# Kernel optimization log

Hardware: AMD Instinct MI355X
Metric: run time of the kernel (lower is better)

The kernel has to match this reference:

```python
import jax, jax.numpy as jnp
import numpy as np

VIEW_NUM = 360
CHAN_NUM = 512
BATCH = 2
IMG = 512


def setup_inputs() -> dict:
    key = jax.random.key(0)
    x = jax.random.normal(key, (BATCH, 1, IMG, IMG), dtype=jnp.float32)
    return {"x": x}


def _bilinear_sample_zeros(img, ix, iy):
    """Bilinear sample img (B,1,H,W) at pixel coords ix, iy (H,W), zeros padding.
    Matches F.grid_sample(mode='bilinear', padding_mode='zeros', align_corners=False)."""
    H, W = img.shape[-2], img.shape[-1]
    x0 = jnp.floor(ix)
    y0 = jnp.floor(iy)
    x1 = x0 + 1.0
    y1 = y0 + 1.0
    wx1 = ix - x0
    wx0 = 1.0 - wx1
    wy1 = iy - y0
    wy0 = 1.0 - wy1

    def gather(yy, xx):
        valid = (xx >= 0) & (xx <= W - 1) & (yy >= 0) & (yy <= H - 1)
        xi = jnp.clip(xx, 0, W - 1).astype(jnp.int32)
        yi = jnp.clip(yy, 0, H - 1).astype(jnp.int32)
        # fancy-index over spatial dims -> (B,1,H,W)
        return img[:, :, yi, xi] * valid.astype(img.dtype)

    return (gather(y0, x0) * (wy0 * wx0)
            + gather(y0, x1) * (wy0 * wx1)
            + gather(y1, x0) * (wy1 * wx0)
            + gather(y1, x1) * (wy1 * wx1))


def _fp(x):
    B, C, H, W = x.shape
    # affine_grid base coords, align_corners=False: (2i+1)/N - 1
    bx = (2.0 * jnp.arange(W, dtype=x.dtype) + 1.0) / W - 1.0
    by = (2.0 * jnp.arange(H, dtype=x.dtype) + 1.0) / H - 1.0
    X = bx[None, :]  # (1,W)
    Y = by[:, None]  # (H,1)
    i = jnp.arange(VIEW_NUM, dtype=x.dtype)
    angles = -jnp.pi * (i + 1.0) / VIEW_NUM - jnp.pi
    cosv = jnp.cos(angles)
    sinv = jnp.sin(angles)

    def per_view(carry, cs):
        c, s = cs
        # theta = [[c,-s,0],[s,c,0]]; grid = base @ theta^T
        gx = c * X - s * Y  # (H,W) normalized sample x
        gy = s * X + c * Y  # (H,W) normalized sample y
        # unnormalize (align_corners=False)
        ix = ((gx + 1.0) * W - 1.0) * 0.5
        iy = ((gy + 1.0) * H - 1.0) * 0.5
        samp = _bilinear_sample_zeros(x, ix, iy)  # (B,1,H,W)
        return carry, jnp.sum(samp, axis=2)  # sum over height -> (B,1,W)

    _, cols = jax.lax.scan(per_view, 0, (cosv, sinv))  # (V,B,1,W)
    sino = jnp.transpose(cols, (1, 2, 3, 0)) * 0.5  # (B,1,chanNum,viewNum)
    return sino


def reference(x):
    return _fp(x)
```

## Files before the change

### kernel.cpp

```cpp
#include <hip/hip_runtime.h>

typedef __fp16 h2 __attribute__((ext_vector_type(2)));

constexpr int VIEWS = 360;
constexpr int IMGSZ = 512;
constexpr int WCHUNK = 64;
constexpr int KH = 64;
constexpr int NXF4 = 25;
constexpr int PITCH = 100;
constexpr int MAXNY = 94;
constexpr int PW = 712;
constexpr int PH = 704;
constexpr int PAD = 96;

__global__ __launch_bounds__(256) void pad_kernel(const float* __restrict__ x,
                                                  unsigned* __restrict__ padq) {
    constexpr int PW4 = PW / 4;
    constexpr int total = PH * PW4;
    int idx = blockIdx.x * 256 + threadIdx.x;
    if (idx >= total) return;
    int py = idx / PW4;
    int px4 = idx - py * PW4;
    int gx = px4 * 4 - PAD;
    int gy = py - PAD;
    const float* img0 = x;
    const float* img1 = x + (size_t)IMGSZ * IMGSZ;
    float4 a = make_float4(0.f, 0.f, 0.f, 0.f);
    float4 bq = a;
    if ((unsigned)gy < (unsigned)IMGSZ && (unsigned)gx < (unsigned)IMGSZ) {
        size_t off = (size_t)gy * IMGSZ + gx;
        a  = *(const float4*)(img0 + off);
        bq = *(const float4*)(img1 + off);
    }
    uint4 d;
    d.x = __builtin_bit_cast(unsigned, __builtin_amdgcn_cvt_pkrtz(a.x, bq.x));
    d.y = __builtin_bit_cast(unsigned, __builtin_amdgcn_cvt_pkrtz(a.y, bq.y));
    d.z = __builtin_bit_cast(unsigned, __builtin_amdgcn_cvt_pkrtz(a.z, bq.z));
    d.w = __builtin_bit_cast(unsigned, __builtin_amdgcn_cvt_pkrtz(a.w, bq.w));
    *(uint4*)&padq[(size_t)idx * 4] = d;
}

__global__ __launch_bounds__(256) void fp_kernel(const unsigned* __restrict__ padq,
                                                 float* __restrict__ out) {
    __shared__ __align__(16) unsigned tileU[PITCH * MAXNY];

    int blk = blockIdx.x;
    int wc = blk & 7;
    int v = blk >> 3;

    int tid = threadIdx.x;
    int lane = tid & 63;
    int g = tid >> 6;
    int w = wc * WCHUNK + lane;

    double ang = -3.14159265358979323846 * (double)(v + 1) / (double)VIEWS
                 - 3.14159265358979323846;
    float c = (float)cos(ang);
    float s = (float)sin(ang);

    float xw = (float)w + 0.5f - 256.0f;
    float cxw = fmaf(c, xw, 255.5f);
    float sxw = fmaf(s, xw, 255.5f);

    float lo = -1e30f, hi = 1e30f;
    {
        float coef = -s, base = cxw;
        if (fabsf(coef) > 1e-6f) {
            float a = (-1.0f - base) / coef;
            float bq = (512.0f - base) / coef;
            lo = fmaxf(lo, fminf(a, bq));
            hi = fminf(hi, fmaxf(a, bq));
        } else if (!(base > -1.0f && base < 512.0f)) {
            lo = 1e30f; hi = -1e30f;
        }
    }
    {
        float coef = c, base = sxw;
        if (fabsf(coef) > 1e-6f) {
            float a = (-1.0f - base) / coef;
            float bq = (512.0f - base) / coef;
            lo = fmaxf(lo, fminf(a, bq));
            hi = fminf(hi, fmaxf(a, bq));
        } else if (!(base > -1.0f && base < 512.0f)) {
            lo = 1e30f; hi = -1e30f;
        }
    }
    float h0f = fminf(fmaxf(floorf(lo + 255.5f) - 1.0f, 0.0f), 512.0f);
    float h1f = fminf(fmaxf(ceilf(hi + 255.5f) + 1.0f, -1.0f), 511.0f);
    int h0 = (int)h0f;
    int h1 = (int)h1f;

    int bh0 = h0, bh1 = h1;
    #pragma unroll
    for (int m = 1; m < 64; m <<= 1) {
        bh0 = min(bh0, __shfl_xor(bh0, m, 64));
        bh1 = max(bh1, __shfl_xor(bh1, m, 64));
    }

    float xa = (float)(wc * WCHUNK) + 0.5f - 256.0f;
    float xb = xa + 63.0f;

    float acc0 = 0.0f, acc1 = 0.0f;
    float step4x = -4.0f * s;
    float step4y = 4.0f * c;

    for (int hc = bh0; hc <= bh1; hc += KH) {
        int hend = min(hc + KH - 1, bh1);

        float ha = (float)hc - 255.5f;
        float hb = (float)hend - 255.5f;
        float ix00 = c * xa - s * ha, ix01 = c * xa - s * hb;
        float ix10 = c * xb - s * ha, ix11 = c * xb - s * hb;
        float iy00 = s * xa + c * ha, iy01 = s * xa + c * hb;
        float iy10 = s * xb + c * ha, iy11 = s * xb + c * hb;
        float ixmn = fminf(fminf(ix00, ix01), fminf(ix10, ix11)) + 255.5f;
        float iymn = fminf(fminf(iy00, iy01), fminf(iy10, iy11)) + 255.5f;
        float iymx = fmaxf(fmaxf(iy00, iy01), fmaxf(iy10, iy11)) + 255.5f;
        int x_lo = (int)floorf(ixmn) - 1;
        int x_lo4 = x_lo & ~3;
        int y_lo = (int)floorf(iymn) - 1;
        int NY = min((int)floorf(iymx) + 3 - y_lo, MAXNY);
        int total4 = NY * NXF4;
        int nit = (total4 + 255) >> 8;

        __syncthreads();

        {
            const unsigned* pb = padq + (y_lo + PAD) * PW + (x_lo4 + PAD);
            for (int k = 0; k < nit; ++k) {
                int i = (k << 8) + tid;
                int ic = min(i, total4 - 1);
                int ry = ic / NXF4;
                uint4 val = *(const uint4*)(pb + 4 * ic + (PW - 4 * NXF4) * ry);
                *(uint4*)&tileU[ic << 2] = val;
            }
        }
        __syncthreads();

        float hh0 = (float)(hc + g) - 255.5f;
        float ixr = fmaf(-s, hh0, cxw) - (float)x_lo4;
        float iyr = fmaf(c, hh0, sxw) - (float)y_lo;
        h2 accp0 = (h2)0.0f;
        h2 accp1 = (h2)0.0f;
        int parity = 0;
        #pragma unroll 4
        for (int h = hc + g; h <= hend; h += 4) {
            float fx = floorf(ixr);
            float fy = floorf(iyr);
            int lx = (int)fx;
            int ly = (int)fy;
            float wx1 = ixr - fx;
            float wy1 = iyr - fy;
            h2 wxs = __builtin_amdgcn_cvt_pkrtz(wx1, wx1);
            h2 wys = __builtin_amdgcn_cvt_pkrtz(wy1, wy1);
            const unsigned* p = tileU + (ly * PITCH + lx);
            h2 t00 = __builtin_bit_cast(h2, p[0]);
            h2 t01 = __builtin_bit_cast(h2, p[1]);
            h2 t10 = __builtin_bit_cast(h2, p[PITCH]);
            h2 t11 = __builtin_bit_cast(h2, p[PITCH + 1]);
            h2 r0 = t00 + (t01 - t00) * wxs;
            h2 r1 = t10 + (t11 - t10) * wxs;
            h2 contrib = r0 + (r1 - r0) * wys;
            if (parity) accp1 += contrib; else accp0 += contrib;
            parity ^= 1;
            ixr += step4x;
            iyr += step4y;
        }
        acc0 += (float)accp0.x + (float)accp1.x;
        acc1 += (float)accp0.y + (float)accp1.y;
    }

    __syncthreads();
    tileU[(g << 6) + lane] = __float_as_uint(acc0);
    tileU[256 + (g << 6) + lane] = __float_as_uint(acc1);
    __syncthreads();
    if (g == 0) {
        float r0 = __uint_as_float(tileU[lane]) + __uint_as_float(tileU[64 + lane]) +
                   __uint_as_float(tileU[128 + lane]) + __uint_as_float(tileU[192 + lane]);
        float r1 = __uint_as_float(tileU[256 + lane]) + __uint_as_float(tileU[320 + lane]) +
                   __uint_as_float(tileU[384 + lane]) + __uint_as_float(tileU[448 + lane]);
        size_t o = (size_t)w * VIEWS + v;
        out[o] = r0 * 0.5f;
        out[(size_t)IMGSZ * VIEWS + o] = r1 * 0.5f;
    }
}

extern "C" void kernel_launch(void* const* d_in, const int* in_sizes, int n_in,
                              void* d_out, int out_size, void* d_ws, size_t ws_size,
                              hipStream_t stream) {
    const float* x = (const float*)d_in[0];
    float* out = (float*)d_out;
    unsigned* padq = (unsigned*)d_ws;

    constexpr int padTotal = PH * (PW / 4);
    pad_kernel<<<(padTotal + 255) / 256, 256, 0, stream>>>(x, padq);

    int nblocks = VIEWS * (IMGSZ / WCHUNK);
    fp_kernel<<<nblocks, 256, 0, stream>>>(padq, out);
}
```

Baseline: 153.7 us.

## Narrow column chunk to 32 and split height across 8 thread phases

```diff
diff --git a/kernel.cpp b/kernel.cpp
--- a/kernel.cpp
+++ b/kernel.cpp
@@ -4,11 +4,11 @@
 
 constexpr int VIEWS = 360;
 constexpr int IMGSZ = 512;
-constexpr int WCHUNK = 64;
+constexpr int WCHUNK = 32;
 constexpr int KH = 64;
-constexpr int NXF4 = 25;
-constexpr int PITCH = 100;
-constexpr int MAXNY = 94;
+constexpr int NXF4 = 20;
+constexpr int PITCH = 82;
+constexpr int MAXNY = 75;
 constexpr int PW = 712;
 constexpr int PH = 704;
 constexpr int PAD = 96;
@@ -45,13 +45,15 @@
     __shared__ __align__(16) unsigned tileU[PITCH * MAXNY];
 
     int blk = blockIdx.x;
-    int wc = blk & 7;
-    int v = blk >> 3;
+    int wc = blk & 15;
+    int v = blk >> 4;
 
     int tid = threadIdx.x;
     int lane = tid & 63;
     int g = tid >> 6;
-    int w = wc * WCHUNK + lane;
+    int lw = lane & 31;
+    int ph = (g << 1) | (lane >> 5);
+    int w = wc * WCHUNK + lw;
 
     double ang = -3.14159265358979323846 * (double)(v + 1) / (double)VIEWS
                  - 3.14159265358979323846;
@@ -98,11 +100,11 @@
     }
 
     float xa = (float)(wc * WCHUNK) + 0.5f - 256.0f;
-    float xb = xa + 63.0f;
+    float xb = xa + 31.0f;
 
     float acc0 = 0.0f, acc1 = 0.0f;
-    float step4x = -4.0f * s;
-    float step4y = 4.0f * c;
+    float step8x = -8.0f * s;
+    float step8y = 8.0f * c;
 
     for (int hc = bh0; hc <= bh1; hc += KH) {
         int hend = min(hc + KH - 1, bh1);
@@ -131,20 +133,23 @@
                 int i = (k << 8) + tid;
                 int ic = min(i, total4 - 1);
                 int ry = ic / NXF4;
+                int rx4 = ic - ry * NXF4;
                 uint4 val = *(const uint4*)(pb + 4 * ic + (PW - 4 * NXF4) * ry);
-                *(uint4*)&tileU[ic << 2] = val;
+                int la = ry * PITCH + (rx4 << 2);
+                *(uint2*)&tileU[la]     = make_uint2(val.x, val.y);
+                *(uint2*)&tileU[la + 2] = make_uint2(val.z, val.w);
             }
         }
         __syncthreads();
 
-        float hh0 = (float)(hc + g) - 255.5f;
+        float hh0 = (float)(hc + ph) - 255.5f;
         float ixr = fmaf(-s, hh0, cxw) - (float)x_lo4;
         float iyr = fmaf(c, hh0, sxw) - (float)y_lo;
         h2 accp0 = (h2)0.0f;
         h2 accp1 = (h2)0.0f;
         int parity = 0;
         #pragma unroll 4
-        for (int h = hc + g; h <= hend; h += 4) {
+        for (int h = hc + ph; h <= hend; h += 8) {
             float fx = floorf(ixr);
             float fy = floorf(iyr);
             int lx = (int)fx;
@@ -163,25 +168,27 @@
             h2 contrib = r0 + (r1 - r0) * wys;
             if (parity) accp1 += contrib; else accp0 += contrib;
             parity ^= 1;
-            ixr += step4x;
-            iyr += step4y;
+            ixr += step8x;
+            iyr += step8y;
         }
         acc0 += (float)accp0.x + (float)accp1.x;
         acc1 += (float)accp0.y + (float)accp1.y;
     }
 
     __syncthreads();
-    tileU[(g << 6) + lane] = __float_as_uint(acc0);
-    tileU[256 + (g << 6) + lane] = __float_as_uint(acc1);
+    tileU[(ph << 5) + lw] = __float_as_uint(acc0);
+    tileU[256 + (ph << 5) + lw] = __float_as_uint(acc1);
     __syncthreads();
-    if (g == 0) {
-        float r0 = __uint_as_float(tileU[lane]) + __uint_as_float(tileU[64 + lane]) +
-                   __uint_as_float(tileU[128 + lane]) + __uint_as_float(tileU[192 + lane]);
-        float r1 = __uint_as_float(tileU[256 + lane]) + __uint_as_float(tileU[320 + lane]) +
-                   __uint_as_float(tileU[384 + lane]) + __uint_as_float(tileU[448 + lane]);
-        size_t o = (size_t)w * VIEWS + v;
-        out[o] = r0 * 0.5f;
-        out[(size_t)IMGSZ * VIEWS + o] = r1 * 0.5f;
+    if (tid < 64) {
+        int lwr = tid & 31;
+        int bsel = tid >> 5;
+        const unsigned* base = tileU + bsel * 256;
+        float r = 0.0f;
+        #pragma unroll
+        for (int k = 0; k < 8; ++k)
+            r += __uint_as_float(base[(k << 5) + lwr]);
+        size_t o = (size_t)(wc * WCHUNK + lwr) * VIEWS + v;
+        out[(size_t)bsel * IMGSZ * VIEWS + o] = r * 0.5f;
     }
 }
 
```

Result: slower. 168.9 us (+9.9%).

## Use transposed padded image for steep view angles to shrink staged tiles

Applied to the files above, without the earlier changes.

```diff
diff --git a/kernel.cpp b/kernel.cpp
--- a/kernel.cpp
+++ b/kernel.cpp
@@ -11,10 +11,13 @@
 constexpr int MAXNY = 94;
 constexpr int PW = 712;
 constexpr int PH = 704;
+constexpr int PWT = 704;
 constexpr int PAD = 96;
+constexpr size_t PADQ_DW = (size_t)PH * PW;
 
 __global__ __launch_bounds__(256) void pad_kernel(const float* __restrict__ x,
-                                                  unsigned* __restrict__ padq) {
+                                                  unsigned* __restrict__ padq,
+                                                  unsigned* __restrict__ padT) {
     constexpr int PW4 = PW / 4;
     constexpr int total = PH * PW4;
     int idx = blockIdx.x * 256 + threadIdx.x;
@@ -38,9 +41,15 @@
     d.z = __builtin_bit_cast(unsigned, __builtin_amdgcn_cvt_pkrtz(a.z, bq.z));
     d.w = __builtin_bit_cast(unsigned, __builtin_amdgcn_cvt_pkrtz(a.w, bq.w));
     *(uint4*)&padq[(size_t)idx * 4] = d;
+    unsigned dd[4] = {d.x, d.y, d.z, d.w};
+    int px = px4 * 4;
+    #pragma unroll
+    for (int j = 0; j < 4; ++j)
+        if (px + j < PWT) padT[(size_t)(px + j) * PWT + py] = dd[j];
 }
 
 __global__ __launch_bounds__(256) void fp_kernel(const unsigned* __restrict__ padq,
+                                                 const unsigned* __restrict__ padT,
                                                  float* __restrict__ out) {
     __shared__ __align__(16) unsigned tileU[PITCH * MAXNY];
 
@@ -58,13 +67,21 @@
     float c = (float)cos(ang);
     float s = (float)sin(ang);
 
+    bool useB = fabsf(s) > fabsf(c);
+    float uc = useB ? s : c;
+    float us = useB ? c : -s;
+    float tc = useB ? c : s;
+    float ts = useB ? -s : c;
+    const unsigned* basePad = useB ? padT : padq;
+    int PWsel = useB ? PWT : PW;
+
     float xw = (float)w + 0.5f - 256.0f;
-    float cxw = fmaf(c, xw, 255.5f);
-    float sxw = fmaf(s, xw, 255.5f);
+    float cu = fmaf(uc, xw, 255.5f);
+    float ct = fmaf(tc, xw, 255.5f);
 
     float lo = -1e30f, hi = 1e30f;
     {
-        float coef = -s, base = cxw;
+        float coef = us, base = cu;
         if (fabsf(coef) > 1e-6f) {
             float a = (-1.0f - base) / coef;
             float bq = (512.0f - base) / coef;
@@ -75,7 +92,7 @@
         }
     }
     {
-        float coef = c, base = sxw;
+        float coef = ts, base = ct;
         if (fabsf(coef) > 1e-6f) {
             float a = (-1.0f - base) / coef;
             float bq = (512.0f - base) / coef;
@@ -101,70 +118,70 @@
     float xb = xa + 63.0f;
 
     float acc0 = 0.0f, acc1 = 0.0f;
-    float step4x = -4.0f * s;
-    float step4y = 4.0f * c;
+    float step4u = 4.0f * us;
+    float step4t = 4.0f * ts;
 
     for (int hc = bh0; hc <= bh1; hc += KH) {
         int hend = min(hc + KH - 1, bh1);
 
         float ha = (float)hc - 255.5f;
         float hb = (float)hend - 255.5f;
-        float ix00 = c * xa - s * ha, ix01 = c * xa - s * hb;
-        float ix10 = c * xb - s * ha, ix11 = c * xb - s * hb;
-        float iy00 = s * xa + c * ha, iy01 = s * xa + c * hb;
-        float iy10 = s * xb + c * ha, iy11 = s * xb + c * hb;
-        float ixmn = fminf(fminf(ix00, ix01), fminf(ix10, ix11)) + 255.5f;
-        float iymn = fminf(fminf(iy00, iy01), fminf(iy10, iy11)) + 255.5f;
-        float iymx = fmaxf(fmaxf(iy00, iy01), fmaxf(iy10, iy11)) + 255.5f;
-        int x_lo = (int)floorf(ixmn) - 1;
-        int x_lo4 = x_lo & ~3;
-        int y_lo = (int)floorf(iymn) - 1;
-        int NY = min((int)floorf(iymx) + 3 - y_lo, MAXNY);
+        float u00 = uc * xa + us * ha, u01 = uc * xa + us * hb;
+        float u10 = uc * xb + us * ha, u11 = uc * xb + us * hb;
+        float t00c = tc * xa + ts * ha, t01c = tc * xa + ts * hb;
+        float t10c = tc * xb + ts * ha, t11c = tc * xb + ts * hb;
+        float umn = fminf(fminf(u00, u01), fminf(u10, u11)) + 255.5f;
+        float tmn = fminf(fminf(t00c, t01c), fminf(t10c, t11c)) + 255.5f;
+        float tmx = fmaxf(fmaxf(t00c, t01c), fmaxf(t10c, t11c)) + 255.5f;
+        int u_lo = (int)floorf(umn) - 1;
+        int u_lo4 = u_lo & ~3;
+        int t_lo = (int)floorf(tmn) - 1;
+        int NY = min((int)floorf(tmx) + 3 - t_lo, MAXNY);
         int total4 = NY * NXF4;
         int nit = (total4 + 255) >> 8;
 
         __syncthreads();
 
         {
-            const unsigned* pb = padq + (y_lo + PAD) * PW + (x_lo4 + PAD);
+            const unsigned* pb = basePad + (t_lo + PAD) * PWsel + (u_lo4 + PAD);
             for (int k = 0; k < nit; ++k) {
                 int i = (k << 8) + tid;
                 int ic = min(i, total4 - 1);
                 int ry = ic / NXF4;
-                uint4 val = *(const uint4*)(pb + 4 * ic + (PW - 4 * NXF4) * ry);
+                uint4 val = *(const uint4*)(pb + 4 * ic + (PWsel - 4 * NXF4) * ry);
                 *(uint4*)&tileU[ic << 2] = val;
             }
         }
         __syncthreads();
 
         float hh0 = (float)(hc + g) - 255.5f;
-        float ixr = fmaf(-s, hh0, cxw) - (float)x_lo4;
-        float iyr = fmaf(c, hh0, sxw) - (float)y_lo;
+        float ur = fmaf(us, hh0, cu) - (float)u_lo4;
+        float tr = fmaf(ts, hh0, ct) - (float)t_lo;
         h2 accp0 = (h2)0.0f;
         h2 accp1 = (h2)0.0f;
         int parity = 0;
         #pragma unroll 4
         for (int h = hc + g; h <= hend; h += 4) {
-            float fx = floorf(ixr);
-            float fy = floorf(iyr);
-            int lx = (int)fx;
-            int ly = (int)fy;
-            float wx1 = ixr - fx;
-            float wy1 = iyr - fy;
-            h2 wxs = __builtin_amdgcn_cvt_pkrtz(wx1, wx1);
-            h2 wys = __builtin_amdgcn_cvt_pkrtz(wy1, wy1);
-            const unsigned* p = tileU + (ly * PITCH + lx);
+            float fu = floorf(ur);
+            float ft = floorf(tr);
+            int lu = (int)fu;
+            int lt = (int)ft;
+            float wu1 = ur - fu;
+            float wt1 = tr - ft;
+            h2 wus = __builtin_amdgcn_cvt_pkrtz(wu1, wu1);
+            h2 wts = __builtin_amdgcn_cvt_pkrtz(wt1, wt1);
+            const unsigned* p = tileU + (lt * PITCH + lu);
             h2 t00 = __builtin_bit_cast(h2, p[0]);
             h2 t01 = __builtin_bit_cast(h2, p[1]);
             h2 t10 = __builtin_bit_cast(h2, p[PITCH]);
             h2 t11 = __builtin_bit_cast(h2, p[PITCH + 1]);
-            h2 r0 = t00 + (t01 - t00) * wxs;
-            h2 r1 = t10 + (t11 - t10) * wxs;
-            h2 contrib = r0 + (r1 - r0) * wys;
+            h2 r0 = t00 + (t01 - t00) * wus;
+            h2 r1 = t10 + (t11 - t10) * wus;
+            h2 contrib = r0 + (r1 - r0) * wts;
             if (parity) accp1 += contrib; else accp0 += contrib;
             parity ^= 1;
-            ixr += step4x;
-            iyr += step4y;
+            ur += step4u;
+            tr += step4t;
         }
         acc0 += (float)accp0.x + (float)accp1.x;
         acc1 += (float)accp0.y + (float)accp1.y;
@@ -191,10 +208,11 @@
     const float* x = (const float*)d_in[0];
     float* out = (float*)d_out;
     unsigned* padq = (unsigned*)d_ws;
+    unsigned* padT = padq + PADQ_DW;
 
     constexpr int padTotal = PH * (PW / 4);
-    pad_kernel<<<(padTotal + 255) / 256, 256, 0, stream>>>(x, padq);
+    pad_kernel<<<(padTotal + 255) / 256, 256, 0, stream>>>(x, padq, padT);
 
     int nblocks = VIEWS * (IMGSZ / WCHUNK);
-    fp_kernel<<<nblocks, 256, 0, stream>>>(padq, out);
+    fp_kernel<<<nblocks, 256, 0, stream>>>(padq, padT, out);
 }
```

Result: slower. 159.3 us (+3.7%).
